# Kernel tuning notes

Hardware: AMD Instinct MI355X
Metric: run time of the kernel (lower is better)

Reference implementation:

```python
import jax, jax.numpy as jnp
import numpy as np

N = 8192
NFEAT = 512
NHID = 512
NCLASS = 8
EPS = 1e-9
ADJ_P = 0.01  # edge density


def setup_inputs() -> dict:
    key = jax.random.key(0)
    ks = jax.random.split(key, 16)
    adj = (jax.random.uniform(ks[0], (N, N)) < ADJ_P).astype(jnp.float32)
    x = jax.random.normal(ks[1], (N, NFEAT), dtype=jnp.float32)
    s_in = 1.0 / np.sqrt(NFEAT)
    s_h = 1.0 / np.sqrt(NHID)
    return {
        "adj": adj,
        "x": x,
        "gcn1_W": jax.random.normal(ks[2], (NFEAT, NHID), jnp.float32) * s_in,
        "gcn1_b": jnp.zeros((NHID,), jnp.float32),
        "Qw": jax.random.normal(ks[3], (NHID, NHID), jnp.float32) * s_h,
        "Qb": jnp.zeros((NHID,), jnp.float32),
        "Kw": jax.random.normal(ks[4], (NHID, NHID), jnp.float32) * s_h,
        "Kb": jnp.zeros((NHID,), jnp.float32),
        "Vw": jax.random.normal(ks[5], (NHID, NHID), jnp.float32) * s_h,
        "Vb": jnp.zeros((NHID,), jnp.float32),
        "ln_g": jnp.ones((NHID,), jnp.float32),
        "ln_b": jnp.zeros((NHID,), jnp.float32),
        "gcn2_W": jax.random.normal(ks[6], (NHID, NCLASS), jnp.float32) * s_h,
        "gcn2_b": jnp.zeros((NCLASS,), jnp.float32),
    }


def _gcn_norm(a):
    # symmetric degree normalization D^{-1/2} A D^{-1/2}, degrees = row sums
    d_inv_sqrt = jax.lax.rsqrt(a.sum(axis=1) + EPS)  # [N]
    return d_inv_sqrt[:, None] * a * d_inv_sqrt[None, :]


def _layer_norm(x, g, b):
    mu = x.mean(axis=-1, keepdims=True)
    var = x.var(axis=-1, keepdims=True)
    return (x - mu) * jax.lax.rsqrt(var + 1e-5) * g + b


def reference(adj, x, gcn1_W, gcn1_b, Qw, Qb, Kw, Kb, Vw, Vb, ln_g, ln_b, gcn2_W, gcn2_b):
    # GraphConvolution: adj @ (x W) + b, then ReLU
    h = jax.nn.relu(adj @ (x @ gcn1_W) + gcn1_b)  # [N, NHID]
    Qh = h @ Qw + Qb
    Kh = h @ Kw + Kb
    Vh = h @ Vw + Vb
    # adjacency-masked dense scores (multiplicative mask, as in original)
    A_tilde = adj * (Qh @ Kh.T)  # [N, N]
    attention = jax.nn.softmax(A_tilde, axis=1)
    X_tilde = _gcn_norm(attention) @ Vh  # [N, NHID]
    X_tilde = _layer_norm(X_tilde, ln_g, ln_b)
    z = adj @ (X_tilde @ gcn2_W) + gcn2_b  # [N, NCLASS]
    return jax.nn.softmax(z, axis=1)
```

## Files before the change

### kernel.cpp

```cpp
#include <hip/hip_runtime.h>
#include <math.h>

#define N_NODES 8192
#define NFEAT 512
#define NHID 512
#define NCLASS 8
#define RCAP 192
#define KB_SPLIT 1536
#define KA_SPLIT 1024
#define CANDCAP 64
#define FILTER_MARGIN 96.0f
#define SROWS 4

__device__ inline ushort f2bf(float f) {
  uint32_t u = __float_as_uint(f);
  uint32_t r = u + 0x7fffu + ((u >> 16) & 1u);
  return (ushort)(r >> 16);
}
__device__ inline float bf2f(ushort h) { return __uint_as_float(((uint32_t)h) << 16); }

__global__ __launch_bounds__(256) void build_ell(const float* __restrict__ adj,
                                                 int* __restrict__ colidx,
                                                 int* __restrict__ deg) {
  int row = blockIdx.x;
  __shared__ int cnt;
  __shared__ int cols[RCAP];
  if (threadIdx.x == 0) cnt = 0;
  __syncthreads();
  const float4* arow = (const float4*)(adj + (size_t)row * N_NODES);
#pragma unroll
  for (int it = 0; it < N_NODES / 4 / 256; ++it) {
    int i = it * 256 + threadIdx.x;
    float4 v = arow[i];
    int base = i * 4;
    if (v.x > 0.5f) { int p = atomicAdd(&cnt, 1); if (p < RCAP) cols[p] = base; }
    if (v.y > 0.5f) { int p = atomicAdd(&cnt, 1); if (p < RCAP) cols[p] = base + 1; }
    if (v.z > 0.5f) { int p = atomicAdd(&cnt, 1); if (p < RCAP) cols[p] = base + 2; }
    if (v.w > 0.5f) { int p = atomicAdd(&cnt, 1); if (p < RCAP) cols[p] = base + 3; }
    __syncthreads();
  }
  int d = cnt < RCAP ? cnt : RCAP;
  if (threadIdx.x == 0) deg[row] = d;
  for (int i = threadIdx.x; i < d; i += 256) colidx[(size_t)row * RCAP + i] = cols[i];
}

__global__ void transpose512(const float* __restrict__ in, float* __restrict__ out) {
  __shared__ float tile[32][33];
  int x = blockIdx.x * 32 + threadIdx.x;
  int y0 = blockIdx.y * 32;
  for (int i = threadIdx.y; i < 32; i += 8)
    tile[i][threadIdx.x] = in[(size_t)(y0 + i) * 512 + x];
  __syncthreads();
  int xo = blockIdx.y * 32 + threadIdx.x;
  int yo0 = blockIdx.x * 32;
  for (int i = threadIdx.y; i < 32; i += 8)
    out[(size_t)(yo0 + i) * 512 + xo] = tile[threadIdx.x][i];
}

__global__ __launch_bounds__(256) void sgemm64x128(const float* __restrict__ A,
                                                   const float* __restrict__ B,
                                                   float* __restrict__ C,
                                                   int M, int Nn, int K, int ldc) {
  __shared__ float As[16][68];
  __shared__ float Bs[16][132];
  const int tid = threadIdx.x;
  const int bm = blockIdx.y * 64, bn = blockIdx.x * 128;
  const int tx = tid & 15, ty = tid >> 4;
  const int arow = tid >> 2, acol = (tid & 3) << 2;
  const int brow = tid >> 4, bcol = (tid & 15) << 2;
  float acc[4][8];
#pragma unroll
  for (int i = 0; i < 4; ++i)
#pragma unroll
    for (int j = 0; j < 8; ++j) acc[i][j] = 0.f;
  const float* Ap = A + (size_t)(bm + arow) * K + acol;
  const float* Bp = B + (size_t)brow * Nn + bn + bcol;
  float4 av = *(const float4*)(Ap);
  float4 bv0 = *(const float4*)(Bp);
  float4 bv1 = *(const float4*)(Bp + 64);
  for (int k0 = 0; k0 < K; k0 += 16) {
    if (k0) __syncthreads();
    As[acol + 0][arow] = av.x;
    As[acol + 1][arow] = av.y;
    As[acol + 2][arow] = av.z;
    As[acol + 3][arow] = av.w;
    *(float4*)&Bs[brow][bcol] = bv0;
    *(float4*)&Bs[brow][bcol + 64] = bv1;
    __syncthreads();
    int kn = (k0 + 16 < K) ? k0 + 16 : 0;
    av = *(const float4*)(Ap + kn);
    bv0 = *(const float4*)(Bp + (size_t)kn * Nn);
    bv1 = *(const float4*)(Bp + (size_t)kn * Nn + 64);
#pragma unroll
    for (int kk = 0; kk < 16; ++kk) {
      float4 a = *(const float4*)&As[kk][ty << 2];
      float4 b0 = *(const float4*)&Bs[kk][tx << 2];
      float4 b1 = *(const float4*)&Bs[kk][(tx << 2) + 64];
      float ar[4] = {a.x, a.y, a.z, a.w};
      float br[8] = {b0.x, b0.y, b0.z, b0.w, b1.x, b1.y, b1.z, b1.w};
#pragma unroll
      for (int i = 0; i < 4; ++i)
#pragma unroll
        for (int j = 0; j < 8; ++j) acc[i][j] = fmaf(ar[i], br[j], acc[i][j]);
    }
  }
#pragma unroll
  for (int i = 0; i < 4; ++i) {
    int r = bm + (ty << 2) + i;
    *(float4*)(C + (size_t)r * ldc + bn + (tx << 2)) =
        make_float4(acc[i][0], acc[i][1], acc[i][2], acc[i][3]);
    *(float4*)(C + (size_t)r * ldc + bn + 64 + (tx << 2)) =
        make_float4(acc[i][4], acc[i][5], acc[i][6], acc[i][7]);
  }
}

__global__ __launch_bounds__(256) void split_a2(const float* __restrict__ A, ushort* __restrict__ As) {
  int idx = blockIdx.x * 256 + threadIdx.x;
  int m = idx >> 7, t = idx & 127;
  float4 v = ((const float4*)(A + (size_t)m * 512))[t];
  ushort4 hi, lo;
  hi.x = f2bf(v.x); hi.y = f2bf(v.y); hi.z = f2bf(v.z); hi.w = f2bf(v.w);
  lo.x = f2bf(v.x - bf2f(hi.x)); lo.y = f2bf(v.y - bf2f(hi.y));
  lo.z = f2bf(v.z - bf2f(hi.z)); lo.w = f2bf(v.w - bf2f(hi.w));
  ushort* row = As + (size_t)m * KA_SPLIT;
  ((ushort4*)row)[t] = hi;
  ((ushort4*)(row + 512))[t] = lo;
}

__global__ __launch_bounds__(256) void split_bt(const float* __restrict__ B, ushort* __restrict__ Bt, int Nn) {
  int idx = blockIdx.x * 256 + threadIdx.x;
  int n = idx / 384, t = idx % 384;
  int sec = t >> 7;
  int k0 = (t & 127) << 2;
  ushort4 o;
  float f0 = B[(size_t)(k0 + 0) * Nn + n];
  float f1 = B[(size_t)(k0 + 1) * Nn + n];
  float f2 = B[(size_t)(k0 + 2) * Nn + n];
  float f3 = B[(size_t)(k0 + 3) * Nn + n];
  if (sec == 1) {
    o.x = f2bf(f0 - bf2f(f2bf(f0))); o.y = f2bf(f1 - bf2f(f2bf(f1)));
    o.z = f2bf(f2 - bf2f(f2bf(f2))); o.w = f2bf(f3 - bf2f(f2bf(f3)));
  } else {
    o.x = f2bf(f0); o.y = f2bf(f1); o.z = f2bf(f2); o.w = f2bf(f3);
  }
  ((ushort4*)(Bt + (size_t)n * KB_SPLIT))[t] = o;
}

__global__ __launch_bounds__(256) void split_bt_cat(const float* __restrict__ Mm, const float* __restrict__ Vw,
                                                    ushort* __restrict__ Bt) {
  int idx = blockIdx.x * 256 + threadIdx.x;
  int n = idx / 384, t = idx % 384;
  const float* src = (n < 512) ? (Mm + n) : (Vw + (n - 512));
  int sec = t >> 7;
  int k0 = (t & 127) << 2;
  ushort4 o;
  float f0 = src[(size_t)(k0 + 0) * 512];
  float f1 = src[(size_t)(k0 + 1) * 512];
  float f2 = src[(size_t)(k0 + 2) * 512];
  float f3 = src[(size_t)(k0 + 3) * 512];
  if (sec == 1) {
    o.x = f2bf(f0 - bf2f(f2bf(f0))); o.y = f2bf(f1 - bf2f(f2bf(f1)));
    o.z = f2bf(f2 - bf2f(f2bf(f2))); o.w = f2bf(f3 - bf2f(f2bf(f3)));
  } else {
    o.x = f2bf(f0); o.y = f2bf(f1); o.z = f2bf(f2); o.w = f2bf(f3);
  }
  ((ushort4*)(Bt + (size_t)n * KB_SPLIT))[t] = o;
}

__global__ void prep_misc(const float* __restrict__ Vb, float* __restrict__ bcat,
                          float* __restrict__ T) {
  int i = blockIdx.x * 256 + threadIdx.x;
  if (i < 1024) bcat[i] = (i < 512) ? 0.f : Vb[i - 512];
  else if (i < 1536) T[i - 1024] = 0.f;
}

using frag_ab = __attribute__((ext_vector_type(8))) short;
using frag_cd = __attribute__((ext_vector_type(4))) float;

__global__ __launch_bounds__(256) void mfma_gemm_bt(const ushort* __restrict__ A,
                                                    const ushort* __restrict__ Bt,
                                                    const float* __restrict__ bias,
                                                    float* __restrict__ C,
                                                    int ldc, float* __restrict__ Tsum) {
  __shared__ __align__(16) ushort Atile[128 * 64];
  __shared__ __align__(16) ushort Btile[128 * 64];
  const int tid = threadIdx.x;
  const int w = tid >> 6, lane = tid & 63;
  const int m0 = blockIdx.y * 128, n0 = blockIdx.x * 128;
  const int wm = (w >> 1) * 64, wn = (w & 1) * 64;
  const int q = lane >> 4, c16 = lane & 15;

  frag_cd acc[4][4];
#pragma unroll
  for (int i = 0; i < 4; ++i)
#pragma unroll
    for (int j = 0; j < 4; ++j) acc[i][j] = (frag_cd){0.f, 0.f, 0.f, 0.f};

  const int srow = (w << 3) + (lane >> 3);
  const int scolb = (lane & 7) << 4;
  const uint8_t* gA = (const uint8_t*)A + (size_t)(m0 + srow) * (KA_SPLIT * 2) + scolb;
  const uint8_t* gB = (const uint8_t*)Bt + (size_t)(n0 + srow) * (KB_SPLIT * 2) + scolb;

  for (int c = 0; c < 24; ++c) {
    const size_t kaB = (size_t)((c < 8 ? c : c - 8) * 128);
    const size_t kbB = (size_t)(c * 128);
#pragma unroll
    for (int r = 0; r < 4; ++r) {
      __builtin_amdgcn_global_load_lds(
          (const __attribute__((address_space(1))) uint32_t*)(gA + (size_t)(r * 32) * (KA_SPLIT * 2) + kaB),
          (__attribute__((address_space(3))) uint32_t*)((uint8_t*)Atile + r * 4096 + w * 1024), 16, 0, 0);
      __builtin_amdgcn_global_load_lds(
          (const __attribute__((address_space(1))) uint32_t*)(gB + (size_t)(r * 32) * (KB_SPLIT * 2) + kbB),
          (__attribute__((address_space(3))) uint32_t*)((uint8_t*)Btile + r * 4096 + w * 1024), 16, 0, 0);
    }
    __syncthreads();
#pragma unroll
    for (int kk = 0; kk < 2; ++kk) {
      frag_ab af[4], bf[4];
#pragma unroll
      for (int i = 0; i < 4; ++i) {
        af[i] = *(const frag_ab*)((const uint8_t*)Atile + (wm + i * 16 + c16) * 128 + kk * 64 + q * 16);
        bf[i] = *(const frag_ab*)((const uint8_t*)Btile + (wn + i * 16 + c16) * 128 + kk * 64 + q * 16);
      }
#pragma unroll
      for (int i = 0; i < 4; ++i)
#pragma unroll
        for (int j = 0; j < 4; ++j)
          acc[i][j] = __builtin_amdgcn_mfma_f32_16x16x32_bf16(af[i], bf[j], acc[i][j], 0, 0, 0);
    }
    __syncthreads();
  }
#pragma unroll
  for (int j = 0; j < 4; ++j) {
    int col = n0 + wn + j * 16 + c16;
    float bv = bias ? bias[col] : 0.f;
    float csum = 0.f;
#pragma unroll
    for (int i = 0; i < 4; ++i) {
      int row = m0 + wm + i * 16 + q * 4;
#pragma unroll
      for (int r = 0; r < 4; ++r) {
        float v = acc[i][j][r] + bv;
        C[(size_t)(row + r) * ldc + col] = v;
        csum += v;
      }
    }
    if (Tsum && col >= 512) {
      csum += __shfl_xor(csum, 16, 64);
      csum += __shfl_xor(csum, 32, 64);
      if (q == 0) atomicAdd(&Tsum[col - 512], csum);
    }
  }
}

__global__ __launch_bounds__(64) void bias_prep(const float* __restrict__ Qw, const float* __restrict__ Kw,
                                                const float* __restrict__ Qb, const float* __restrict__ Kb,
                                                float* __restrict__ u, float* __restrict__ w,
                                                float* __restrict__ cbuf) {
  int k = blockIdx.x;
  int lane = threadIdx.x;
  if (k == NHID) {
    float s = 0.f;
    for (int j = lane; j < NHID; j += 64) s = fmaf(Qb[j], Kb[j], s);
#pragma unroll
    for (int o = 32; o > 0; o >>= 1) s += __shfl_down(s, o, 64);
    if (lane == 0) cbuf[0] = s;
    return;
  }
  float su = 0.f, sw = 0.f;
  for (int j = lane; j < NHID; j += 64) {
    su = fmaf(Qw[(size_t)k * NHID + j], Kb[j], su);
    sw = fmaf(Kw[(size_t)k * NHID + j], Qb[j], sw);
  }
#pragma unroll
  for (int o = 32; o > 0; o >>= 1) { su += __shfl_down(su, o, 64); sw += __shfl_down(sw, o, 64); }
  if (lane == 0) { u[k] = su; w[k] = sw; }
}

__global__ __launch_bounds__(128) void spmm_persist(const float* __restrict__ xW,
                                                    const int* __restrict__ colidx,
                                                    const int* __restrict__ deg,
                                                    const float* __restrict__ b1,
                                                    const float* __restrict__ u, const float* __restrict__ w,
                                                    float* __restrict__ h, ushort* __restrict__ Hs,
                                                    float* __restrict__ a_vec, float* __restrict__ b_vec) {
  __shared__ int scols[SROWS][RCAP];
  __shared__ float ra[2], rb[2];
  int t = threadIdx.x;
  int row0 = blockIdx.x * SROWS;
  int d[SROWS];
#pragma unroll
  for (int r = 0; r < SROWS; ++r) {
    d[r] = deg[row0 + r];
    for (int i = t; i < d[r]; i += 128) scols[r][i] = colidx[(size_t)(row0 + r) * RCAP + i];
  }
  __syncthreads();
  float4 bv = ((const float4*)b1)[t];
  float4 uv = ((const float4*)u)[t], wv4 = ((const float4*)w)[t];
  int wid = t >> 6, lane = t & 63;
#pragma unroll
  for (int r = 0; r < SROWS; ++r) {
    int row = row0 + r;
    int dd = d[r];
    float4 acc = make_float4(0.f, 0.f, 0.f, 0.f);
    int e = 0;
    for (; e + 8 <= dd; e += 8) {
      float4 v0 = ((const float4*)(xW + (size_t)scols[r][e + 0] * NHID))[t];
      float4 v1 = ((const float4*)(xW + (size_t)scols[r][e + 1] * NHID))[t];
      float4 v2 = ((const float4*)(xW + (size_t)scols[r][e + 2] * NHID))[t];
      float4 v3 = ((const float4*)(xW + (size_t)scols[r][e + 3] * NHID))[t];
      float4 v4 = ((const float4*)(xW + (size_t)scols[r][e + 4] * NHID))[t];
      float4 v5 = ((const float4*)(xW + (size_t)scols[r][e + 5] * NHID))[t];
      float4 v6 = ((const float4*)(xW + (size_t)scols[r][e + 6] * NHID))[t];
      float4 v7 = ((const float4*)(xW + (size_t)scols[r][e + 7] * NHID))[t];
      acc.x += ((v0.x + v1.x) + (v2.x + v3.x)) + ((v4.x + v5.x) + (v6.x + v7.x));
      acc.y += ((v0.y + v1.y) + (v2.y + v3.y)) + ((v4.y + v5.y) + (v6.y + v7.y));
      acc.z += ((v0.z + v1.z) + (v2.z + v3.z)) + ((v4.z + v5.z) + (v6.z + v7.z));
      acc.w += ((v0.w + v1.w) + (v2.w + v3.w)) + ((v4.w + v5.w) + (v6.w + v7.w));
    }
    for (; e < dd; ++e) {
      float4 v = ((const float4*)(xW + (size_t)scols[r][e] * NHID))[t];
      acc.x += v.x; acc.y += v.y; acc.z += v.z; acc.w += v.w;
    }
    float4 o = make_float4(fmaxf(acc.x + bv.x, 0.f), fmaxf(acc.y + bv.y, 0.f),
                           fmaxf(acc.z + bv.z, 0.f), fmaxf(acc.w + bv.w, 0.f));
    ((float4*)(h + (size_t)row * NHID))[t] = o;
    ushort4 hi, lo;
    hi.x = f2bf(o.x); hi.y = f2bf(o.y); hi.z = f2bf(o.z); hi.w = f2bf(o.w);
    lo.x = f2bf(o.x - bf2f(hi.x)); lo.y = f2bf(o.y - bf2f(hi.y));
    lo.z = f2bf(o.z - bf2f(hi.z)); lo.w = f2bf(o.w - bf2f(hi.w));
    ushort* hr = Hs + (size_t)row * KA_SPLIT;
    ((ushort4*)hr)[t] = hi;
    ((ushort4*)(hr + 512))[t] = lo;
    float sa = fmaf(o.x, uv.x, fmaf(o.y, uv.y, fmaf(o.z, uv.z, o.w * uv.w)));
    float sb = fmaf(o.x, wv4.x, fmaf(o.y, wv4.y, fmaf(o.z, wv4.z, o.w * wv4.w)));
#pragma unroll
    for (int off = 32; off > 0; off >>= 1) { sa += __shfl_down(sa, off, 64); sb += __shfl_down(sb, off, 64); }
    if (lane == 0) { ra[wid] = sa; rb[wid] = sb; }
    __syncthreads();
    if (t == 0) { a_vec[row] = ra[0] + ra[1]; b_vec[row] = rb[0] + rb[1]; }
    __syncthreads();
  }
}

__global__ __launch_bounds__(256) void score2_agg_ln(
    const float* __restrict__ G, int ldg, const float* __restrict__ h,
    const ushort* __restrict__ Hs, const int* __restrict__ colidx, const int* __restrict__ deg,
    const float* __restrict__ a_vec, const float* __restrict__ b_vec,
    const float* __restrict__ cbuf, const float* __restrict__ Vh, int ldv,
    const float* __restrict__ T, const float* __restrict__ lng,
    const float* __restrict__ lnb, const float* __restrict__ W2, float* __restrict__ Y) {
  __shared__ int scols[4][RCAP];
  __shared__ float sbv[4][RCAP];
  __shared__ float sv[4][RCAP];
  __shared__ int cand[4][CANDCAP];
  __shared__ int ccnt[4];
  __shared__ float w2s[NHID * NCLASS];
  int t = threadIdx.x, wv = t >> 6, lane = t & 63;
  int row = blockIdx.x * 4 + wv;
  int d = deg[row];
  int q = lane >> 4, u = lane & 15;
  for (int i = t; i < NHID * NCLASS; i += 256) w2s[i] = W2[i];
  if (lane == 0) ccnt[wv] = 0;
  float4 ga4[4][2];
  const float4* Gr4 = (const float4*)(G + (size_t)row * ldg);
#pragma unroll
  for (int it2 = 0; it2 < 4; ++it2) {
    ga4[it2][0] = Gr4[it2 * 32 + 2 * u];
    ga4[it2][1] = Gr4[it2 * 32 + 2 * u + 1];
  }
  for (int i = lane; i < d; i += 64) {
    int c = colidx[(size_t)row * RCAP + i];
    scols[wv][i] = c;
    sbv[wv][i] = b_vec[c];
  }
  __syncthreads();
  for (int e0 = 0; e0 < d; e0 += 4) {
    int e = e0 + q;
    bool act = e < d;
    int col = scols[wv][act ? e : 0];
    const uint4* hr = (const uint4*)(Hs + (size_t)col * KA_SPLIT);
    float s_a = 0.f, s_b = 0.f;
#pragma unroll
    for (int it2 = 0; it2 < 4; ++it2) {
      uint4 p = hr[it2 * 16 + u];
      float4 g0 = ga4[it2][0], g1 = ga4[it2][1];
      s_a = fmaf(__uint_as_float(p.x << 16), g0.x, s_a);
      s_a = fmaf(__uint_as_float(p.x & 0xffff0000u), g0.y, s_a);
      s_a = fmaf(__uint_as_float(p.y << 16), g0.z, s_a);
      s_a = fmaf(__uint_as_float(p.y & 0xffff0000u), g0.w, s_a);
      s_b = fmaf(__uint_as_float(p.z << 16), g1.x, s_b);
      s_b = fmaf(__uint_as_float(p.z & 0xffff0000u), g1.y, s_b);
      s_b = fmaf(__uint_as_float(p.w << 16), g1.z, s_b);
      s_b = fmaf(__uint_as_float(p.w & 0xffff0000u), g1.w, s_b);
    }
    float s = s_a + s_b;
    s += __shfl_down(s, 8, 16);
    s += __shfl_down(s, 4, 16);
    s += __shfl_down(s, 2, 16);
    s += __shfl_down(s, 1, 16);
    if (u == 0 && act) sv[wv][e] = s + sbv[wv][e];
  }
  __syncthreads();
  float fm = -1e30f;
  for (int i = lane; i < d; i += 64) fm = fmaxf(fm, sv[wv][i]);
#pragma unroll
  for (int o = 32; o > 0; o >>= 1) fm = fmaxf(fm, __shfl_xor(fm, o, 64));
  for (int i = lane; i < d; i += 64) {
    if (sv[wv][i] >= fm - FILTER_MARGIN) {
      int p = atomicAdd(&ccnt[wv], 1);
      if (p < CANDCAP) cand[wv][p] = i;
    }
  }
  __syncthreads();
  int nc = ccnt[wv];
  bool ovf = nc > CANDCAP;
  if (ovf) nc = d;
  float ai = a_vec[row] + cbuf[0];
  for (int c0 = 0; c0 < nc; c0 += 4) {
    int idx = c0 + q;
    bool act = idx < nc;
    int e = act ? (ovf ? idx : cand[wv][idx]) : 0;
    int col = scols[wv][e];
    const float4* hr = (const float4*)(h + (size_t)col * NHID);
    float s_a = 0.f, s_b = 0.f;
#pragma unroll
    for (int it2 = 0; it2 < 4; ++it2) {
      float4 h0 = hr[it2 * 32 + 2 * u], h1 = hr[it2 * 32 + 2 * u + 1];
      float4 g0 = ga4[it2][0], g1 = ga4[it2][1];
      s_a = fmaf(h0.x, g0.x, s_a); s_a = fmaf(h0.y, g0.y, s_a);
      s_a = fmaf(h0.z, g0.z, s_a); s_a = fmaf(h0.w, g0.w, s_a);
      s_b = fmaf(h1.x, g1.x, s_b); s_b = fmaf(h1.y, g1.y, s_b);
      s_b = fmaf(h1.z, g1.z, s_b); s_b = fmaf(h1.w, g1.w, s_b);
    }
    float s = s_a + s_b;
    s += __shfl_down(s, 8, 16);
    s += __shfl_down(s, 4, 16);
    s += __shfl_down(s, 2, 16);
    s += __shfl_down(s, 1, 16);
    if (u == 0 && act) sv[wv][e] = s + ai + sbv[wv][e];
  }
  __syncthreads();
  float m = 0.f;
  for (int i = lane; i < nc; i += 64) {
    int e = ovf ? i : cand[wv][i];
    m = fmaxf(m, sv[wv][e]);
  }
#pragma unroll
  for (int o = 32; o > 0; o >>= 1) m = fmaxf(m, __shfl_xor(m, o, 64));
  float ssum = 0.f;
  for (int i = lane; i < nc; i += 64) {
    int e = ovf ? i : cand[wv][i];
    float ex = expf(sv[wv][e] - m);
    sv[wv][e] = ex;
    ssum += ex;
  }
#pragma unroll
  for (int o = 32; o > 0; o >>= 1) ssum += __shfl_xor(ssum, o, 64);
  float em = expf(-m);
  float inv = 1.f / (ssum + (float)(N_NODES - d) * em);
  float ci = em * inv;
  __syncthreads();
  float4 a0 = make_float4(0.f, 0.f, 0.f, 0.f), a1 = a0;
  for (int i = 0; i < nc; ++i) {
    int e = ovf ? i : cand[wv][i];
    float we = sv[wv][e] * inv;
    if (we > 1e-12f) {
      const float4* vr = (const float4*)(Vh + (size_t)scols[wv][e] * ldv);
      float4 v0 = vr[lane * 2], v1 = vr[lane * 2 + 1];
      a0.x = fmaf(we, v0.x, a0.x); a0.y = fmaf(we, v0.y, a0.y);
      a0.z = fmaf(we, v0.z, a0.z); a0.w = fmaf(we, v0.w, a0.w);
      a1.x = fmaf(we, v1.x, a1.x); a1.y = fmaf(we, v1.y, a1.y);
      a1.z = fmaf(we, v1.z, a1.z); a1.w = fmaf(we, v1.w, a1.w);
    }
  }
  float4 t0 = ((const float4*)T)[lane * 2], t1 = ((const float4*)T)[lane * 2 + 1];
  a0.x = fmaf(ci, t0.x, a0.x); a0.y = fmaf(ci, t0.y, a0.y);
  a0.z = fmaf(ci, t0.z, a0.z); a0.w = fmaf(ci, t0.w, a0.w);
  a1.x = fmaf(ci, t1.x, a1.x); a1.y = fmaf(ci, t1.y, a1.y);
  a1.z = fmaf(ci, t1.z, a1.z); a1.w = fmaf(ci, t1.w, a1.w);
  float s1 = ((a0.x + a0.y) + (a0.z + a0.w)) + ((a1.x + a1.y) + (a1.z + a1.w));
  float s2 = ((a0.x * a0.x + a0.y * a0.y) + (a0.z * a0.z + a0.w * a0.w)) +
             ((a1.x * a1.x + a1.y * a1.y) + (a1.z * a1.z + a1.w * a1.w));
#pragma unroll
  for (int o = 32; o > 0; o >>= 1) { s1 += __shfl_xor(s1, o, 64); s2 += __shfl_xor(s2, o, 64); }
  float mu = s1 * (1.f / NHID);
  float var = s2 * (1.f / NHID) - mu * mu;
  float rstd = rsqrtf(var + 1e-5f);
  float4 g0 = ((const float4*)lng)[lane * 2], g1 = ((const float4*)lng)[lane * 2 + 1];
  float4 b0 = ((const float4*)lnb)[lane * 2], b1v = ((const float4*)lnb)[lane * 2 + 1];
  float4 o0, o1;
  o0.x = (a0.x - mu) * rstd * g0.x + b0.x;
  o0.y = (a0.y - mu) * rstd * g0.y + b0.y;
  o0.z = (a0.z - mu) * rstd * g0.z + b0.z;
  o0.w = (a0.w - mu) * rstd * g0.w + b0.w;
  o1.x = (a1.x - mu) * rstd * g1.x + b1v.x;
  o1.y = (a1.y - mu) * rstd * g1.y + b1v.y;
  o1.z = (a1.z - mu) * rstd * g1.z + b1v.z;
  o1.w = (a1.w - mu) * rstd * g1.w + b1v.w;
  float xv[8] = {o0.x, o0.y, o0.z, o0.w, o1.x, o1.y, o1.z, o1.w};
  float accc[NCLASS];
#pragma unroll
  for (int c = 0; c < NCLASS; ++c) accc[c] = 0.f;
#pragma unroll
  for (int kk = 0; kk < 8; ++kk) {
    int k = lane * 8 + kk;
#pragma unroll
    for (int c = 0; c < NCLASS; ++c) accc[c] = fmaf(xv[kk], w2s[k * NCLASS + c], accc[c]);
  }
#pragma unroll
  for (int c = 0; c < NCLASS; ++c)
#pragma unroll
    for (int o = 32; o > 0; o >>= 1) accc[c] += __shfl_down(accc[c], o, 64);
  if (lane == 0) {
    *(float4*)(Y + (size_t)row * NCLASS) = make_float4(accc[0], accc[1], accc[2], accc[3]);
    *(float4*)(Y + (size_t)row * NCLASS + 4) = make_float4(accc[4], accc[5], accc[6], accc[7]);
  }
}

__global__ __launch_bounds__(256) void final_spmm_softmax(const float* __restrict__ Y,
                                                          const int* __restrict__ colidx,
                                                          const int* __restrict__ deg,
                                                          const float* __restrict__ b2,
                                                          float* __restrict__ out) {
  int t = threadIdx.x;
  int wv = t >> 6, lane = t & 63;
  int row = blockIdx.x * 4 + wv;
  int d = deg[row];
  const int* cols = colidx + (size_t)row * RCAP;
  float acc[8];
#pragma unroll
  for (int c = 0; c < 8; ++c) acc[c] = 0.f;
  for (int e = lane; e < d; e += 64) {
    int col = cols[e];
    const float4* yr = (const float4*)(Y + (size_t)col * 8);
    float4 y0 = yr[0], y1 = yr[1];
    acc[0] += y0.x; acc[1] += y0.y; acc[2] += y0.z; acc[3] += y0.w;
    acc[4] += y1.x; acc[5] += y1.y; acc[6] += y1.z; acc[7] += y1.w;
  }
#pragma unroll
  for (int c = 0; c < 8; ++c)
#pragma unroll
    for (int o = 32; o > 0; o >>= 1) acc[c] += __shfl_down(acc[c], o, 64);
  if (lane == 0) {
    float z[8];
    float m = -1e30f;
#pragma unroll
    for (int c = 0; c < 8; ++c) { z[c] = acc[c] + b2[c]; m = fmaxf(m, z[c]); }
    float s = 0.f;
#pragma unroll
    for (int c = 0; c < 8; ++c) { z[c] = expf(z[c] - m); s += z[c]; }
    float inv = 1.f / s;
    *(float4*)(out + (size_t)row * 8) = make_float4(z[0] * inv, z[1] * inv, z[2] * inv, z[3] * inv);
    *(float4*)(out + (size_t)row * 8 + 4) = make_float4(z[4] * inv, z[5] * inv, z[6] * inv, z[7] * inv);
  }
}

extern "C" void kernel_launch(void* const* d_in, const int* in_sizes, int n_in,
                              void* d_out, int out_size, void* d_ws, size_t ws_size,
                              hipStream_t stream) {
  const float* adj = (const float*)d_in[0];
  const float* x = (const float*)d_in[1];
  const float* W1 = (const float*)d_in[2];
  const float* b1 = (const float*)d_in[3];
  const float* Qw = (const float*)d_in[4];
  const float* Qb = (const float*)d_in[5];
  const float* Kw = (const float*)d_in[6];
  const float* Kb = (const float*)d_in[7];
  const float* Vw = (const float*)d_in[8];
  const float* Vb = (const float*)d_in[9];
  const float* ln_g = (const float*)d_in[10];
  const float* ln_b = (const float*)d_in[11];
  const float* W2 = (const float*)d_in[12];
  const float* b2 = (const float*)d_in[13];
  float* out = (float*)d_out;

  char* ws = (char*)d_ws;
  size_t off = 0;
  auto alloc = [&](size_t bytes) -> void* {
    void* p = ws + off;
    off = (off + bytes + 255) & ~(size_t)255;
    return p;
  };
  int* colidx = (int*)alloc((size_t)N_NODES * RCAP * 4);
  int* deg = (int*)alloc((size_t)N_NODES * 4);
  float* bufA = (float*)alloc((size_t)N_NODES * NHID * 4);
  float* bufB = (float*)alloc((size_t)N_NODES * NHID * 4);
  float* GVh = (float*)alloc((size_t)N_NODES * 1024 * 4);
  ushort* Xs = (ushort*)alloc((size_t)N_NODES * KA_SPLIT * 2);
  ushort* Hs = (ushort*)alloc((size_t)N_NODES * KA_SPLIT * 2);
  ushort* W1ts = (ushort*)alloc((size_t)512 * KB_SPLIT * 2);
  ushort* Bcts = (ushort*)alloc((size_t)1024 * KB_SPLIT * 2);
  float* KwT = (float*)alloc((size_t)512 * 512 * 4);
  float* Mmat = (float*)alloc((size_t)512 * 512 * 4);
  float* bcat = (float*)alloc((size_t)1024 * 4);
  float* a_vec = (float*)alloc((size_t)N_NODES * 4);
  float* b_vec = (float*)alloc((size_t)N_NODES * 4);
  float* u_vec = (float*)alloc((size_t)NHID * 4);
  float* w_vec = (float*)alloc((size_t)NHID * 4);
  float* cbuf = (float*)alloc(256);
  float* T = (float*)alloc((size_t)NHID * 4);
  float* Y = (float*)alloc((size_t)N_NODES * NCLASS * 4);
  (void)in_sizes; (void)n_in; (void)out_size; (void)ws_size;

  build_ell<<<N_NODES, 256, 0, stream>>>(adj, colidx, deg);
  transpose512<<<dim3(16, 16), dim3(32, 8), 0, stream>>>(Kw, KwT);
  bias_prep<<<NHID + 1, 64, 0, stream>>>(Qw, Kw, Qb, Kb, u_vec, w_vec, cbuf);
  sgemm64x128<<<dim3(4, 8), 256, 0, stream>>>(Qw, KwT, Mmat, 512, 512, 512, 512);
  split_a2<<<(N_NODES * 128) / 256, 256, 0, stream>>>(x, Xs);
  split_bt<<<(512 * 384) / 256, 256, 0, stream>>>(W1, W1ts, 512);
  mfma_gemm_bt<<<dim3(4, 64), 256, 0, stream>>>(Xs, W1ts, nullptr, bufA, 512, nullptr);
  spmm_persist<<<N_NODES / SROWS, 128, 0, stream>>>(bufA, colidx, deg, b1, u_vec, w_vec,
                                                    bufB, Hs, a_vec, b_vec);
  split_bt_cat<<<(1024 * 384) / 256, 256, 0, stream>>>(Mmat, Vw, Bcts);
  prep_misc<<<6, 256, 0, stream>>>(Vb, bcat, T);
  mfma_gemm_bt<<<dim3(8, 64), 256, 0, stream>>>(Hs, Bcts, bcat, GVh, 1024, T);
  score2_agg_ln<<<N_NODES / 4, 256, 0, stream>>>(GVh, 1024, bufB, Hs, colidx, deg, a_vec, b_vec,
                                                 cbuf, GVh + 512, 1024, T, ln_g, ln_b, W2, Y);
  final_spmm_softmax<<<N_NODES / 4, 256, 0, stream>>>(Y, colidx, deg, b2, out);
}
```

Measured before the change: 767.0 us.

## Merge prep kernels into one launch and split SpMM edges across two half-blocks

```diff
diff --git a/kernel.cpp b/kernel.cpp
--- a/kernel.cpp
+++ b/kernel.cpp
@@ -12,6 +12,13 @@
 #define FILTER_MARGIN 96.0f
 #define SROWS 4
 
+#define PB_SPLITA 256
+#define PB_SPLITB (PB_SPLITA + 4096)
+#define PB_SPLITV (PB_SPLITB + 768)
+#define PB_BIAS   (PB_SPLITV + 768)
+#define PB_MISC   (PB_BIAS + 129)
+#define PB_TOTAL  (PB_MISC + 6)
+
 __device__ inline ushort f2bf(float f) {
   uint32_t u = __float_as_uint(f);
   uint32_t r = u + 0x7fffu + ((u >> 16) & 1u);
@@ -44,17 +51,115 @@
   for (int i = threadIdx.x; i < d; i += 256) colidx[(size_t)row * RCAP + i] = cols[i];
 }
 
-__global__ void transpose512(const float* __restrict__ in, float* __restrict__ out) {
+__global__ __launch_bounds__(256) void prep_all(
+    const float* __restrict__ Kw, float* __restrict__ KwT,
+    const float* __restrict__ x, ushort* __restrict__ Xs,
+    const float* __restrict__ W1, ushort* __restrict__ W1ts,
+    const float* __restrict__ Vw, ushort* __restrict__ Bcts,
+    const float* __restrict__ Qw, const float* __restrict__ Qb, const float* __restrict__ Kb,
+    float* __restrict__ u, float* __restrict__ w, float* __restrict__ cbuf,
+    const float* __restrict__ Vb, float* __restrict__ bcat, float* __restrict__ T) {
   __shared__ float tile[32][33];
-  int x = blockIdx.x * 32 + threadIdx.x;
-  int y0 = blockIdx.y * 32;
-  for (int i = threadIdx.y; i < 32; i += 8)
-    tile[i][threadIdx.x] = in[(size_t)(y0 + i) * 512 + x];
-  __syncthreads();
-  int xo = blockIdx.y * 32 + threadIdx.x;
-  int yo0 = blockIdx.x * 32;
-  for (int i = threadIdx.y; i < 32; i += 8)
-    out[(size_t)(yo0 + i) * 512 + xo] = tile[threadIdx.x][i];
+  int b = blockIdx.x, t = threadIdx.x;
+  if (b < PB_SPLITA) {
+    int bx = b & 15, by = b >> 4;
+    int tx = t & 31, ty = t >> 5;
+    int xcol = bx * 32 + tx, y0 = by * 32;
+    for (int i = ty; i < 32; i += 8) tile[i][tx] = Kw[(size_t)(y0 + i) * 512 + xcol];
+    __syncthreads();
+    int xo = by * 32 + tx, yo0 = bx * 32;
+    for (int i = ty; i < 32; i += 8) KwT[(size_t)(yo0 + i) * 512 + xo] = tile[tx][i];
+  } else if (b < PB_SPLITB) {
+    int idx = (b - PB_SPLITA) * 256 + t;
+    int m = idx >> 7, tc = idx & 127;
+    float4 v = ((const float4*)(x + (size_t)m * 512))[tc];
+    ushort4 hi, lo;
+    hi.x = f2bf(v.x); hi.y = f2bf(v.y); hi.z = f2bf(v.z); hi.w = f2bf(v.w);
+    lo.x = f2bf(v.x - bf2f(hi.x)); lo.y = f2bf(v.y - bf2f(hi.y));
+    lo.z = f2bf(v.z - bf2f(hi.z)); lo.w = f2bf(v.w - bf2f(hi.w));
+    ushort* row = Xs + (size_t)m * KA_SPLIT;
+    ((ushort4*)row)[tc] = hi;
+    ((ushort4*)(row + 512))[tc] = lo;
+  } else if (b < PB_SPLITV) {
+    int idx = (b - PB_SPLITB) * 256 + t;
+    int n = idx / 384, tc = idx % 384;
+    int sec = tc >> 7;
+    int k0 = (tc & 127) << 2;
+    ushort4 o;
+    float f0 = W1[(size_t)(k0 + 0) * 512 + n];
+    float f1 = W1[(size_t)(k0 + 1) * 512 + n];
+    float f2 = W1[(size_t)(k0 + 2) * 512 + n];
+    float f3 = W1[(size_t)(k0 + 3) * 512 + n];
+    if (sec == 1) {
+      o.x = f2bf(f0 - bf2f(f2bf(f0))); o.y = f2bf(f1 - bf2f(f2bf(f1)));
+      o.z = f2bf(f2 - bf2f(f2bf(f2))); o.w = f2bf(f3 - bf2f(f2bf(f3)));
+    } else {
+      o.x = f2bf(f0); o.y = f2bf(f1); o.z = f2bf(f2); o.w = f2bf(f3);
+    }
+    ((ushort4*)(W1ts + (size_t)n * KB_SPLIT))[tc] = o;
+  } else if (b < PB_BIAS) {
+    int idx = (b - PB_SPLITV) * 256 + t;
+    int n = idx / 384, tc = idx % 384;
+    const float* src = Vw + n;
+    int sec = tc >> 7;
+    int k0 = (tc & 127) << 2;
+    ushort4 o;
+    float f0 = src[(size_t)(k0 + 0) * 512];
+    float f1 = src[(size_t)(k0 + 1) * 512];
+    float f2 = src[(size_t)(k0 + 2) * 512];
+    float f3 = src[(size_t)(k0 + 3) * 512];
+    if (sec == 1) {
+      o.x = f2bf(f0 - bf2f(f2bf(f0))); o.y = f2bf(f1 - bf2f(f2bf(f1)));
+      o.z = f2bf(f2 - bf2f(f2bf(f2))); o.w = f2bf(f3 - bf2f(f2bf(f3)));
+    } else {
+      o.x = f2bf(f0); o.y = f2bf(f1); o.z = f2bf(f2); o.w = f2bf(f3);
+    }
+    ((ushort4*)(Bcts + (size_t)(512 + n) * KB_SPLIT))[tc] = o;
+  } else if (b < PB_MISC) {
+    int k = (b - PB_BIAS) * 4 + (t >> 6);
+    int lane = t & 63;
+    if (k > NHID) return;
+    if (k == NHID) {
+      float s = 0.f;
+      for (int j = lane; j < NHID; j += 64) s = fmaf(Qb[j], Kb[j], s);
+#pragma unroll
+      for (int o = 32; o > 0; o >>= 1) s += __shfl_down(s, o, 64);
+      if (lane == 0) cbuf[0] = s;
+      return;
+    }
+    float su = 0.f, sw = 0.f;
+    for (int j = lane; j < NHID; j += 64) {
+      su = fmaf(Qw[(size_t)k * NHID + j], Kb[j], su);
+      sw = fmaf(Kw[(size_t)k * NHID + j], Qb[j], sw);
+    }
+#pragma unroll
+    for (int o = 32; o > 0; o >>= 1) { su += __shfl_down(su, o, 64); sw += __shfl_down(sw, o, 64); }
+    if (lane == 0) { u[k] = su; w[k] = sw; }
+  } else {
+    int i = (b - PB_MISC) * 256 + t;
+    if (i < 1024) bcat[i] = (i < 512) ? 0.f : Vb[i - 512];
+    else if (i < 1536) T[i - 1024] = 0.f;
+  }
+}
+
+__global__ __launch_bounds__(256) void split_mmat(const float* __restrict__ Mm, ushort* __restrict__ Bt) {
+  int idx = blockIdx.x * 256 + threadIdx.x;
+  int n = idx / 384, tc = idx % 384;
+  const float* src = Mm + n;
+  int sec = tc >> 7;
+  int k0 = (tc & 127) << 2;
+  ushort4 o;
+  float f0 = src[(size_t)(k0 + 0) * 512];
+  float f1 = src[(size_t)(k0 + 1) * 512];
+  float f2 = src[(size_t)(k0 + 2) * 512];
+  float f3 = src[(size_t)(k0 + 3) * 512];
+  if (sec == 1) {
+    o.x = f2bf(f0 - bf2f(f2bf(f0))); o.y = f2bf(f1 - bf2f(f2bf(f1)));
+    o.z = f2bf(f2 - bf2f(f2bf(f2))); o.w = f2bf(f3 - bf2f(f2bf(f3)));
+  } else {
+    o.x = f2bf(f0); o.y = f2bf(f1); o.z = f2bf(f2); o.w = f2bf(f3);
+  }
+  ((ushort4*)(Bt + (size_t)n * KB_SPLIT))[tc] = o;
 }
 
 __global__ __launch_bounds__(256) void sgemm64x128(const float* __restrict__ A,
@@ -114,66 +219,6 @@
   }
 }
 
-__global__ __launch_bounds__(256) void split_a2(const float* __restrict__ A, ushort* __restrict__ As) {
-  int idx = blockIdx.x * 256 + threadIdx.x;
-  int m = idx >> 7, t = idx & 127;
-  float4 v = ((const float4*)(A + (size_t)m * 512))[t];
-  ushort4 hi, lo;
-  hi.x = f2bf(v.x); hi.y = f2bf(v.y); hi.z = f2bf(v.z); hi.w = f2bf(v.w);
-  lo.x = f2bf(v.x - bf2f(hi.x)); lo.y = f2bf(v.y - bf2f(hi.y));
-  lo.z = f2bf(v.z - bf2f(hi.z)); lo.w = f2bf(v.w - bf2f(hi.w));
-  ushort* row = As + (size_t)m * KA_SPLIT;
-  ((ushort4*)row)[t] = hi;
-  ((ushort4*)(row + 512))[t] = lo;
-}
-
-__global__ __launch_bounds__(256) void split_bt(const float* __restrict__ B, ushort* __restrict__ Bt, int Nn) {
-  int idx = blockIdx.x * 256 + threadIdx.x;
-  int n = idx / 384, t = idx % 384;
-  int sec = t >> 7;
-  int k0 = (t & 127) << 2;
-  ushort4 o;
-  float f0 = B[(size_t)(k0 + 0) * Nn + n];
-  float f1 = B[(size_t)(k0 + 1) * Nn + n];
-  float f2 = B[(size_t)(k0 + 2) * Nn + n];
-  float f3 = B[(size_t)(k0 + 3) * Nn + n];
-  if (sec == 1) {
-    o.x = f2bf(f0 - bf2f(f2bf(f0))); o.y = f2bf(f1 - bf2f(f2bf(f1)));
-    o.z = f2bf(f2 - bf2f(f2bf(f2))); o.w = f2bf(f3 - bf2f(f2bf(f3)));
-  } else {
-    o.x = f2bf(f0); o.y = f2bf(f1); o.z = f2bf(f2); o.w = f2bf(f3);
-  }
-  ((ushort4*)(Bt + (size_t)n * KB_SPLIT))[t] = o;
-}
-
-__global__ __launch_bounds__(256) void split_bt_cat(const float* __restrict__ Mm, const float* __restrict__ Vw,
-                                                    ushort* __restrict__ Bt) {
-  int idx = blockIdx.x * 256 + threadIdx.x;
-  int n = idx / 384, t = idx % 384;
-  const float* src = (n < 512) ? (Mm + n) : (Vw + (n - 512));
-  int sec = t >> 7;
-  int k0 = (t & 127) << 2;
-  ushort4 o;
-  float f0 = src[(size_t)(k0 + 0) * 512];
-  float f1 = src[(size_t)(k0 + 1) * 512];
-  float f2 = src[(size_t)(k0 + 2) * 512];
-  float f3 = src[(size_t)(k0 + 3) * 512];
-  if (sec == 1) {
-    o.x = f2bf(f0 - bf2f(f2bf(f0))); o.y = f2bf(f1 - bf2f(f2bf(f1)));
-    o.z = f2bf(f2 - bf2f(f2bf(f2))); o.w = f2bf(f3 - bf2f(f2bf(f3)));
-  } else {
-    o.x = f2bf(f0); o.y = f2bf(f1); o.z = f2bf(f2); o.w = f2bf(f3);
-  }
-  ((ushort4*)(Bt + (size_t)n * KB_SPLIT))[t] = o;
-}
-
-__global__ void prep_misc(const float* __restrict__ Vb, float* __restrict__ bcat,
-                          float* __restrict__ T) {
-  int i = blockIdx.x * 256 + threadIdx.x;
-  if (i < 1024) bcat[i] = (i < 512) ? 0.f : Vb[i - 512];
-  else if (i < 1536) T[i - 1024] = 0.f;
-}
-
 using frag_ab = __attribute__((ext_vector_type(8))) short;
 using frag_cd = __attribute__((ext_vector_type(4))) float;
 
@@ -253,90 +298,72 @@
   }
 }
 
-__global__ __launch_bounds__(64) void bias_prep(const float* __restrict__ Qw, const float* __restrict__ Kw,
-                                                const float* __restrict__ Qb, const float* __restrict__ Kb,
-                                                float* __restrict__ u, float* __restrict__ w,
-                                                float* __restrict__ cbuf) {
-  int k = blockIdx.x;
-  int lane = threadIdx.x;
-  if (k == NHID) {
-    float s = 0.f;
-    for (int j = lane; j < NHID; j += 64) s = fmaf(Qb[j], Kb[j], s);
-#pragma unroll
-    for (int o = 32; o > 0; o >>= 1) s += __shfl_down(s, o, 64);
-    if (lane == 0) cbuf[0] = s;
-    return;
-  }
-  float su = 0.f, sw = 0.f;
-  for (int j = lane; j < NHID; j += 64) {
-    su = fmaf(Qw[(size_t)k * NHID + j], Kb[j], su);
-    sw = fmaf(Kw[(size_t)k * NHID + j], Qb[j], sw);
-  }
-#pragma unroll
-  for (int o = 32; o > 0; o >>= 1) { su += __shfl_down(su, o, 64); sw += __shfl_down(sw, o, 64); }
-  if (lane == 0) { u[k] = su; w[k] = sw; }
-}
-
-__global__ __launch_bounds__(128) void spmm_persist(const float* __restrict__ xW,
-                                                    const int* __restrict__ colidx,
-                                                    const int* __restrict__ deg,
-                                                    const float* __restrict__ b1,
-                                                    const float* __restrict__ u, const float* __restrict__ w,
-                                                    float* __restrict__ h, ushort* __restrict__ Hs,
-                                                    float* __restrict__ a_vec, float* __restrict__ b_vec) {
+__global__ __launch_bounds__(256, 8) void spmm_persist(const float* __restrict__ xW,
+                                                       const int* __restrict__ colidx,
+                                                       const int* __restrict__ deg,
+                                                       const float* __restrict__ b1,
+                                                       const float* __restrict__ u, const float* __restrict__ w,
+                                                       float* __restrict__ h, ushort* __restrict__ Hs,
+                                                       float* __restrict__ a_vec, float* __restrict__ b_vec) {
   __shared__ int scols[SROWS][RCAP];
+  __shared__ float4 part[128];
   __shared__ float ra[2], rb[2];
-  int t = threadIdx.x;
+  int t = threadIdx.x, half = t >> 7, tt = t & 127;
   int row0 = blockIdx.x * SROWS;
   int d[SROWS];
 #pragma unroll
   for (int r = 0; r < SROWS; ++r) {
     d[r] = deg[row0 + r];
-    for (int i = t; i < d[r]; i += 128) scols[r][i] = colidx[(size_t)(row0 + r) * RCAP + i];
+    for (int i = t; i < d[r]; i += 256) scols[r][i] = colidx[(size_t)(row0 + r) * RCAP + i];
   }
   __syncthreads();
-  float4 bv = ((const float4*)b1)[t];
-  float4 uv = ((const float4*)u)[t], wv4 = ((const float4*)w)[t];
-  int wid = t >> 6, lane = t & 63;
-#pragma unroll
+#pragma unroll 1
   for (int r = 0; r < SROWS; ++r) {
-    int row = row0 + r;
-    int dd = d[r];
+    int row = row0 + r, dd = d[r];
     float4 acc = make_float4(0.f, 0.f, 0.f, 0.f);
-    int e = 0;
-    for (; e + 8 <= dd; e += 8) {
-      float4 v0 = ((const float4*)(xW + (size_t)scols[r][e + 0] * NHID))[t];
-      float4 v1 = ((const float4*)(xW + (size_t)scols[r][e + 1] * NHID))[t];
-      float4 v2 = ((const float4*)(xW + (size_t)scols[r][e + 2] * NHID))[t];
-      float4 v3 = ((const float4*)(xW + (size_t)scols[r][e + 3] * NHID))[t];
-      float4 v4 = ((const float4*)(xW + (size_t)scols[r][e + 4] * NHID))[t];
-      float4 v5 = ((const float4*)(xW + (size_t)scols[r][e + 5] * NHID))[t];
-      float4 v6 = ((const float4*)(xW + (size_t)scols[r][e + 6] * NHID))[t];
-      float4 v7 = ((const float4*)(xW + (size_t)scols[r][e + 7] * NHID))[t];
+    int e = half;
+    for (; e + 14 < dd; e += 16) {
+      float4 v0 = ((const float4*)(xW + (size_t)scols[r][e + 0] * NHID))[tt];
+      float4 v1 = ((const float4*)(xW + (size_t)scols[r][e + 2] * NHID))[tt];
+      float4 v2 = ((const float4*)(xW + (size_t)scols[r][e + 4] * NHID))[tt];
+      float4 v3 = ((const float4*)(xW + (size_t)scols[r][e + 6] * NHID))[tt];
+      float4 v4 = ((const float4*)(xW + (size_t)scols[r][e + 8] * NHID))[tt];
+      float4 v5 = ((const float4*)(xW + (size_t)scols[r][e + 10] * NHID))[tt];
+      float4 v6 = ((const float4*)(xW + (size_t)scols[r][e + 12] * NHID))[tt];
+      float4 v7 = ((const float4*)(xW + (size_t)scols[r][e + 14] * NHID))[tt];
       acc.x += ((v0.x + v1.x) + (v2.x + v3.x)) + ((v4.x + v5.x) + (v6.x + v7.x));
       acc.y += ((v0.y + v1.y) + (v2.y + v3.y)) + ((v4.y + v5.y) + (v6.y + v7.y));
       acc.z += ((v0.z + v1.z) + (v2.z + v3.z)) + ((v4.z + v5.z) + (v6.z + v7.z));
       acc.w += ((v0.w + v1.w) + (v2.w + v3.w)) + ((v4.w + v5.w) + (v6.w + v7.w));
     }
-    for (; e < dd; ++e) {
-      float4 v = ((const float4*)(xW + (size_t)scols[r][e] * NHID))[t];
+    for (; e < dd; e += 2) {
+      float4 v = ((const float4*)(xW + (size_t)scols[r][e] * NHID))[tt];
       acc.x += v.x; acc.y += v.y; acc.z += v.z; acc.w += v.w;
     }
-    float4 o = make_float4(fmaxf(acc.x + bv.x, 0.f), fmaxf(acc.y + bv.y, 0.f),
-                           fmaxf(acc.z + bv.z, 0.f), fmaxf(acc.w + bv.w, 0.f));
-    ((float4*)(h + (size_t)row * NHID))[t] = o;
-    ushort4 hi, lo;
-    hi.x = f2bf(o.x); hi.y = f2bf(o.y); hi.z = f2bf(o.z); hi.w = f2bf(o.w);
-    lo.x = f2bf(o.x - bf2f(hi.x)); lo.y = f2bf(o.y - bf2f(hi.y));
-    lo.z = f2bf(o.z - bf2f(hi.z)); lo.w = f2bf(o.w - bf2f(hi.w));
-    ushort* hr = Hs + (size_t)row * KA_SPLIT;
-    ((ushort4*)hr)[t] = hi;
-    ((ushort4*)(hr + 512))[t] = lo;
-    float sa = fmaf(o.x, uv.x, fmaf(o.y, uv.y, fmaf(o.z, uv.z, o.w * uv.w)));
-    float sb = fmaf(o.x, wv4.x, fmaf(o.y, wv4.y, fmaf(o.z, wv4.z, o.w * wv4.w)));
-#pragma unroll
-    for (int off = 32; off > 0; off >>= 1) { sa += __shfl_down(sa, off, 64); sb += __shfl_down(sb, off, 64); }
-    if (lane == 0) { ra[wid] = sa; rb[wid] = sb; }
+    if (half == 1) part[tt] = acc;
+    __syncthreads();
+    if (half == 0) {
+      float4 p = part[tt];
+      acc.x += p.x; acc.y += p.y; acc.z += p.z; acc.w += p.w;
+      float4 bv = ((const float4*)b1)[tt];
+      float4 o = make_float4(fmaxf(acc.x + bv.x, 0.f), fmaxf(acc.y + bv.y, 0.f),
+                             fmaxf(acc.z + bv.z, 0.f), fmaxf(acc.w + bv.w, 0.f));
+      ((float4*)(h + (size_t)row * NHID))[tt] = o;
+      ushort4 hi, lo;
+      hi.x = f2bf(o.x); hi.y = f2bf(o.y); hi.z = f2bf(o.z); hi.w = f2bf(o.w);
+      lo.x = f2bf(o.x - bf2f(hi.x)); lo.y = f2bf(o.y - bf2f(hi.y));
+      lo.z = f2bf(o.z - bf2f(hi.z)); lo.w = f2bf(o.w - bf2f(hi.w));
+      ushort* hr = Hs + (size_t)row * KA_SPLIT;
+      ((ushort4*)hr)[tt] = hi;
+      ((ushort4*)(hr + 512))[tt] = lo;
+      float4 uv = ((const float4*)u)[tt], wv4 = ((const float4*)w)[tt];
+      float sa = fmaf(o.x, uv.x, fmaf(o.y, uv.y, fmaf(o.z, uv.z, o.w * uv.w)));
+      float sb = fmaf(o.x, wv4.x, fmaf(o.y, wv4.y, fmaf(o.z, wv4.z, o.w * wv4.w)));
+      int wid = tt >> 6, lane = tt & 63;
+#pragma unroll
+      for (int off = 32; off > 0; off >>= 1) { sa += __shfl_down(sa, off, 64); sb += __shfl_down(sb, off, 64); }
+      if (lane == 0) { ra[wid] = sa; rb[wid] = sb; }
+    }
     __syncthreads();
     if (t == 0) { a_vec[row] = ra[0] + ra[1]; b_vec[row] = rb[0] + rb[1]; }
     __syncthreads();
@@ -604,16 +631,13 @@
   (void)in_sizes; (void)n_in; (void)out_size; (void)ws_size;
 
   build_ell<<<N_NODES, 256, 0, stream>>>(adj, colidx, deg);
-  transpose512<<<dim3(16, 16), dim3(32, 8), 0, stream>>>(Kw, KwT);
-  bias_prep<<<NHID + 1, 64, 0, stream>>>(Qw, Kw, Qb, Kb, u_vec, w_vec, cbuf);
+  prep_all<<<PB_TOTAL, 256, 0, stream>>>(Kw, KwT, x, Xs, W1, W1ts, Vw, Bcts,
+                                         Qw, Qb, Kb, u_vec, w_vec, cbuf, Vb, bcat, T);
   sgemm64x128<<<dim3(4, 8), 256, 0, stream>>>(Qw, KwT, Mmat, 512, 512, 512, 512);
-  split_a2<<<(N_NODES * 128) / 256, 256, 0, stream>>>(x, Xs);
-  split_bt<<<(512 * 384) / 256, 256, 0, stream>>>(W1, W1ts, 512);
   mfma_gemm_bt<<<dim3(4, 64), 256, 0, stream>>>(Xs, W1ts, nullptr, bufA, 512, nullptr);
-  spmm_persist<<<N_NODES / SROWS, 128, 0, stream>>>(bufA, colidx, deg, b1, u_vec, w_vec,
+  split_mmat<<<(512 * 384) / 256, 256, 0, stream>>>(Mmat, Bcts);
+  spmm_persist<<<N_NODES / SROWS, 256, 0, stream>>>(bufA, colidx, deg, b1, u_vec, w_vec,
                                                     bufB, Hs, a_vec, b_vec);
-  split_bt_cat<<<(1024 * 384) / 256, 256, 0, stream>>>(Mmat, Vw, Bcts);
-  prep_misc<<<6, 256, 0, stream>>>(Vb, bcat, T);
   mfma_gemm_bt<<<dim3(8, 64), 256, 0, stream>>>(Hs, Bcts, bcat, GVh, 1024, T);
   score2_agg_ln<<<N_NODES / 4, 256, 0, stream>>>(GVh, 1024, bufB, Hs, colidx, deg, a_vec, b_vec,
                                                  cbuf, GVh + 512, 1024, T, ln_g, ln_b, W2, Y);
```

Measured after the change: 757.0 us. Within noise of the previous version (-1.3%).
